# Kernel optimization log

Hardware: AMD Instinct MI355X
Metric: run time of the kernel (lower is better)

## Reference

```python
import jax, jax.numpy as jnp
import numpy as np

D_MODEL = 1024
N_HEADS = 16
D_K = D_MODEL // N_HEADS
SCALE = float(np.sqrt(D_K))


def setup_inputs() -> dict:
    key = jax.random.key(0)
    ks = jax.random.split(key, 12)
    B, S = 2, 2048
    std = 1.0 / np.sqrt(D_MODEL)
    inp = {
        "query": jax.random.normal(ks[0], (B, S, D_MODEL), jnp.float32),
        "key": jax.random.normal(ks[1], (B, S, D_MODEL), jnp.float32),
        "value": jax.random.normal(ks[2], (B, S, D_MODEL), jnp.float32),
        "mask": jnp.ones((B, S), jnp.int32),
        "Wq": jax.random.normal(ks[3], (D_MODEL, D_MODEL), jnp.float32) * std,
        "bq": jnp.zeros((D_MODEL,), jnp.float32),
        "Wk": jax.random.normal(ks[4], (D_MODEL, D_MODEL), jnp.float32) * std,
        "bk": jnp.zeros((D_MODEL,), jnp.float32),
        "Wv": jax.random.normal(ks[5], (D_MODEL, D_MODEL), jnp.float32) * std,
        "bv": jnp.zeros((D_MODEL,), jnp.float32),
        "Wo": jax.random.normal(ks[6], (D_MODEL, D_MODEL), jnp.float32) * std,
        "bo": jnp.zeros((D_MODEL,), jnp.float32),
    }
    return inp


def reference(query, key, value, mask, Wq, bq, Wk, bk, Wv, bv, Wo, bo):
    B, S, _ = query.shape
    # projections -> [B, H, S, d_k]
    def proj(x, W, b):
        return (x @ W.T + b).reshape(B, S, N_HEADS, D_K).transpose(0, 2, 1, 3)

    Q = proj(query, Wq, bq)
    K = proj(key, Wk, bk)
    V = proj(value, Wv, bv)
    # [B, H, Sq, Sk] scores
    scores = jnp.einsum("bhqd,bhkd->bhqk", Q, K) / SCALE
    m = mask[:, None, None, :]  # broadcast over heads and query positions
    scores = jnp.where(m == 0, jnp.float32(-1e9), scores)
    attn = jax.nn.softmax(scores, axis=-1)
    # dropout is identity in eval mode
    context = jnp.einsum("bhqk,bhkd->bhqd", attn, V)
    context = context.transpose(0, 2, 1, 3).reshape(B, S, D_MODEL)
    return context @ Wo.T + bo
```

## Files before the change

### kernel.cpp

```cpp
#include <hip/hip_runtime.h>
#include <stdint.h>

#define D_MODEL 1024
#define NH 16
#define DK 64
#define BATCH 2
#define SEQ 2048
#define MROWS (BATCH*SEQ)

typedef float f32x4 __attribute__((ext_vector_type(4)));
typedef __bf16 bf16x8 __attribute__((ext_vector_type(8)));

#define AS1 __attribute__((address_space(1)))
#define AS3 __attribute__((address_space(3)))

static __device__ __forceinline__ void gld_lds16(const void* g, void* l) {
    __builtin_amdgcn_global_load_lds((const AS1 unsigned int*)g,
                                     (AS3 unsigned int*)l, 16, 0, 0);
}

static __device__ __forceinline__ unsigned int f2bf(float f) {
    union { float f; unsigned int u; } v; v.f = f;
    return (v.u + 0x7fffu + ((v.u >> 16) & 1u)) >> 16;
}

struct PrepArgs {
    const float* src[7];
    unsigned short* dst[7];
    int n4[7];
};

__global__ __launch_bounds__(256) void prep_cvt(PrepArgs a) {
    const int z = blockIdx.y;
    const float4* s = (const float4*)a.src[z];
    ushort4* d = (ushort4*)a.dst[z];
    const int n = a.n4[z];
    for (int i = blockIdx.x * blockDim.x + threadIdx.x; i < n;
         i += gridDim.x * blockDim.x) {
        float4 v = s[i];
        ushort4 o;
        o.x = (unsigned short)f2bf(v.x);
        o.y = (unsigned short)f2bf(v.y);
        o.z = (unsigned short)f2bf(v.z);
        o.w = (unsigned short)f2bf(v.w);
        d[i] = o;
    }
}

struct GemmArgs {
    const unsigned short* A[3];
    const unsigned short* W[3];
    const float* bias[3];
    void* C[3];
    float scale[3];
    int hm[3];
};

template<bool OUT_F32>
__global__ __launch_bounds__(256) void gemm_bt(GemmArgs g) {
    __shared__ unsigned short As[128 * 64];
    __shared__ unsigned short Bs[128 * 64];
    const int z = blockIdx.z;
    const char* A = (const char*)g.A[z];
    const char* W = (const char*)g.W[z];
    const float* bias = g.bias[z];
    const float scale = g.scale[z];
    const int hm = g.hm[z];
    const int t = threadIdx.x;
    const int w = t >> 6, lane = t & 63;
    const int m0 = blockIdx.x * 128, n0 = blockIdx.y * 128;
    const int wm = (w >> 1) * 64, wn = (w & 1) * 64;

    const int srow = t >> 3;
    const int csw = ((t & 7) * 16) ^ ((srow & 7) << 4);
    const char* pA = A + (size_t)(m0 + srow) * 2048 + csw;
    const char* pW = W + (size_t)(n0 + srow) * 2048 + csw;

    f32x4 acc[4][4];
#pragma unroll
    for (int i = 0; i < 4; ++i)
#pragma unroll
        for (int j = 0; j < 4; ++j)
            acc[i][j] = (f32x4){0.f, 0.f, 0.f, 0.f};

    const int kg16 = (lane >> 4) * 16;
    const int swl = (lane & 7) << 4;

    for (int kt = 0; kt < 16; ++kt) {
        __syncthreads();
#pragma unroll
        for (int p = 0; p < 4; ++p) {
            gld_lds16(pA + (size_t)p * (32 * 2048), &As[w * 512 + p * 2048]);
            gld_lds16(pW + (size_t)p * (32 * 2048), &Bs[w * 512 + p * 2048]);
        }
        pA += 128; pW += 128;
        __syncthreads();
#pragma unroll
        for (int ks = 0; ks < 2; ++ks) {
            bf16x8 af[4], bfv[4];
#pragma unroll
            for (int i = 0; i < 4; ++i) {
                int ra = wm + i * 16 + (lane & 15);
                af[i] = *(const bf16x8*)((const char*)As + ra * 128 +
                                         ((ks * 64 + kg16) ^ swl));
                int rb = wn + i * 16 + (lane & 15);
                bfv[i] = *(const bf16x8*)((const char*)Bs + rb * 128 +
                                          ((ks * 64 + kg16) ^ swl));
            }
            __builtin_amdgcn_s_setprio(1);
#pragma unroll
            for (int i = 0; i < 4; ++i)
#pragma unroll
                for (int j = 0; j < 4; ++j)
                    acc[i][j] = __builtin_amdgcn_mfma_f32_16x16x32_bf16(
                        af[i], bfv[j], acc[i][j], 0, 0, 0);
            __builtin_amdgcn_s_setprio(0);
        }
    }

    float bj[4];
#pragma unroll
    for (int j = 0; j < 4; ++j) bj[j] = bias[n0 + wn + j * 16 + (lane & 15)];
#pragma unroll
    for (int i = 0; i < 4; ++i)
#pragma unroll
        for (int r = 0; r < 4; ++r) {
            int row = m0 + wm + i * 16 + (lane >> 4) * 4 + r;
#pragma unroll
            for (int j = 0; j < 4; ++j) {
                int col = n0 + wn + j * 16 + (lane & 15);
                float v = (acc[i][j][r] + bj[j]) * scale;
                if (OUT_F32) {
                    ((float*)g.C[z])[(size_t)row * 1024 + col] = v;
                } else if (hm) {
                    int bb = row >> 11, ss = row & 2047;
                    int hh = col >> 6, dd = col & 63;
                    ((unsigned short*)g.C[z])
                        [(((size_t)(bb * 16 + hh) * 2048) + ss) * 64 + dd] =
                        (unsigned short)f2bf(v);
                } else {
                    ((unsigned short*)g.C[z])[(size_t)row * 1024 + col] =
                        (unsigned short)f2bf(v);
                }
            }
        }
}

__global__ __launch_bounds__(256) void tr_v(
    const unsigned short* __restrict__ Vflat,
    unsigned short* __restrict__ VtT) {
    __shared__ unsigned short T[64 * 66];
    const int bh = blockIdx.y, b = bh >> 4, h = bh & 15;
    const int s0 = blockIdx.x * 64;
    const int t = threadIdx.x, row = t >> 3, ch = t & 7;
#pragma unroll
    for (int p = 0; p < 2; ++p) {
        int r = p * 32 + row;
        const unsigned int* src = (const unsigned int*)(
            Vflat + ((size_t)(b * 2048 + s0 + r) * 1024) + h * 64 + ch * 8);
        unsigned int v0 = src[0], v1 = src[1], v2 = src[2], v3 = src[3];
        unsigned int* dst = (unsigned int*)&T[r * 66 + ch * 8];
        dst[0] = v0; dst[1] = v1; dst[2] = v2; dst[3] = v3;
    }
    __syncthreads();
#pragma unroll
    for (int p = 0; p < 2; ++p) {
        int d = p * 32 + row;
        union { unsigned short u16[8]; uint4 v; } o;
#pragma unroll
        for (int j = 0; j < 8; ++j) o.u16[j] = T[(ch * 8 + j) * 66 + d];
        *(uint4*)(VtT + ((size_t)bh * 64 + d) * 2048 + s0 + ch * 8) = o.v;
    }
}

__global__ __launch_bounds__(256) void attn_fwd(
    const unsigned short* __restrict__ Qh,
    const unsigned short* __restrict__ Kh,
    const unsigned short* __restrict__ VtT,
    const int* __restrict__ mask,
    unsigned short* __restrict__ Ctx) {
    __shared__ unsigned short KlA[4096], KlB[4096];
    __shared__ unsigned short VlA[4096], VlB[4096];
    __shared__ unsigned short Plds[4][2048];

    const int wg = blockIdx.x + (int)gridDim.x * blockIdx.y;
    const int swzid = (wg & 7) * 64 + (wg >> 3);
    const int qt = swzid & 15, bh = swzid >> 4;
    const int b = bh >> 4, h = bh & 15;

    const int t = threadIdx.x, w = t >> 6, lane = t & 63;
    const int wq0 = w * 32;
    const int kg16 = (lane >> 4) * 16;
    const int swl = (lane & 7) << 4;

    const char* Qbase = (const char*)Qh + (size_t)bh * 2048 * 128;
    bf16x8 qf[2][2];
#pragma unroll
    for (int nf = 0; nf < 2; ++nf)
#pragma unroll
        for (int ks = 0; ks < 2; ++ks) {
            int row = qt * 128 + wq0 + nf * 16 + (lane & 15);
            qf[nf][ks] = *(const bf16x8*)(Qbase + (size_t)row * 128 +
                                          ks * 64 + kg16);
        }

    f32x4 cacc[2][4];
#pragma unroll
    for (int i = 0; i < 2; ++i)
#pragma unroll
        for (int j = 0; j < 4; ++j) cacc[i][j] = (f32x4){0.f, 0.f, 0.f, 0.f};
    float mstate[2] = {-3e38f, -3e38f};
    float lstate[2] = {0.f, 0.f};

    const char* Kbyte = (const char*)Kh + (size_t)bh * 2048 * 128;
    const char* Vbyte = (const char*)VtT + (size_t)bh * 64 * 4096;
    const int* mbase = mask + b * SEQ;

    const int srow = t >> 3;
    const int csw = ((t & 7) * 16) ^ ((srow & 7) << 4);
    const size_t srow128 = (size_t)srow * 128;
    const size_t srow4096 = (size_t)srow * 4096;

    auto stage = [&](unsigned short* Kd, unsigned short* Vd, int kv0) {
        const char* ks = Kbyte + (size_t)kv0 * 128;
        gld_lds16(ks + srow128 + csw,               Kd + w * 512);
        gld_lds16(ks + srow128 + 32 * 128 + csw,    Kd + 2048 + w * 512);
        const char* vs = Vbyte + (size_t)kv0 * 2;
        gld_lds16(vs + srow4096 + csw,              Vd + w * 512);
        gld_lds16(vs + srow4096 + 32 * 4096 + csw,  Vd + 2048 + w * 512);
    };

    unsigned short* Pw = &Plds[w][0];

    auto compute = [&](const unsigned short* Kl, const unsigned short* Vl,
                       int kv0) {
        int4 mk[4]; int allone = 1;
#pragma unroll
        for (int mf = 0; mf < 4; ++mf) {
            mk[mf] = *(const int4*)(mbase + kv0 + mf * 16 + (lane >> 4) * 4);
            allone &= (mk[mf].x != 0) & (mk[mf].y != 0) &
                      (mk[mf].z != 0) & (mk[mf].w != 0);
        }

        f32x4 sacc[4][2];
#pragma unroll
        for (int i = 0; i < 4; ++i)
#pragma unroll
            for (int j = 0; j < 2; ++j) sacc[i][j] = (f32x4){0.f, 0.f, 0.f, 0.f};
#pragma unroll
        for (int ks = 0; ks < 2; ++ks) {
            bf16x8 kf[4];
#pragma unroll
            for (int mf = 0; mf < 4; ++mf) {
                int r = mf * 16 + (lane & 15);
                kf[mf] = *(const bf16x8*)((const char*)Kl + r * 128 +
                                          ((ks * 64 + kg16) ^ swl));
            }
            __builtin_amdgcn_s_setprio(1);
#pragma unroll
            for (int mf = 0; mf < 4; ++mf)
#pragma unroll
                for (int nf = 0; nf < 2; ++nf)
                    sacc[mf][nf] = __builtin_amdgcn_mfma_f32_16x16x32_bf16(
                        kf[mf], qf[nf][ks], sacc[mf][nf], 0, 0, 0);
            __builtin_amdgcn_s_setprio(0);
        }

        if (!__all(allone)) {
#pragma unroll
            for (int mf = 0; mf < 4; ++mf)
#pragma unroll
                for (int r = 0; r < 4; ++r) {
                    int mv = (&mk[mf].x)[r];
                    if (mv == 0) {
                        sacc[mf][0][r] = -1e9f;
                        sacc[mf][1][r] = -1e9f;
                    }
                }
        }

        float scalef[2];
#pragma unroll
        for (int nf = 0; nf < 2; ++nf) {
            float a0 = fmaxf(fmaxf(sacc[0][nf][0], sacc[0][nf][1]),
                             fmaxf(sacc[0][nf][2], sacc[0][nf][3]));
            float a1 = fmaxf(fmaxf(sacc[1][nf][0], sacc[1][nf][1]),
                             fmaxf(sacc[1][nf][2], sacc[1][nf][3]));
            float a2 = fmaxf(fmaxf(sacc[2][nf][0], sacc[2][nf][1]),
                             fmaxf(sacc[2][nf][2], sacc[2][nf][3]));
            float a3 = fmaxf(fmaxf(sacc[3][nf][0], sacc[3][nf][1]),
                             fmaxf(sacc[3][nf][2], sacc[3][nf][3]));
            float vm = fmaxf(fmaxf(a0, a1), fmaxf(a2, a3));
            vm = fmaxf(vm, __shfl_xor(vm, 16));
            vm = fmaxf(vm, __shfl_xor(vm, 32));
            float mnew = fmaxf(mstate[nf], vm);
            float sc = __expf(mstate[nf] - mnew);
            scalef[nf] = sc;
            mstate[nf] = mnew;
            float ps[4];
#pragma unroll
            for (int mf = 0; mf < 4; ++mf) {
                float p0 = __expf(sacc[mf][nf][0] - mnew);
                float p1 = __expf(sacc[mf][nf][1] - mnew);
                float p2 = __expf(sacc[mf][nf][2] - mnew);
                float p3 = __expf(sacc[mf][nf][3] - mnew);
                sacc[mf][nf][0] = p0; sacc[mf][nf][1] = p1;
                sacc[mf][nf][2] = p2; sacc[mf][nf][3] = p3;
                ps[mf] = (p0 + p1) + (p2 + p3);
            }
            float s = (ps[0] + ps[1]) + (ps[2] + ps[3]);
            s += __shfl_xor(s, 16);
            s += __shfl_xor(s, 32);
            lstate[nf] = lstate[nf] * sc + s;
        }

#pragma unroll
        for (int mq = 0; mq < 2; ++mq)
#pragma unroll
            for (int r = 0; r < 4; ++r) {
                float sc = __shfl(scalef[mq], (lane >> 4) * 4 + r);
#pragma unroll
                for (int nd = 0; nd < 4; ++nd) cacc[mq][nd][r] *= sc;
            }

#pragma unroll
        for (int nf = 0; nf < 2; ++nf)
#pragma unroll
            for (int mf = 0; mf < 4; ++mf) {
                int q = nf * 16 + (lane & 15);
                int kb = mf * 32 + (lane >> 4) * 8;
                unsigned int p0 = f2bf(sacc[mf][nf][0]) | (f2bf(sacc[mf][nf][1]) << 16);
                unsigned int p1 = f2bf(sacc[mf][nf][2]) | (f2bf(sacc[mf][nf][3]) << 16);
                int sw = (q & 7) << 4;
                *(unsigned int*)((char*)Pw + q * 128 + (kb ^ sw)) = p0;
                *(unsigned int*)((char*)Pw + q * 128 + ((kb + 4) ^ sw)) = p1;
            }

#pragma unroll
        for (int ks = 0; ks < 2; ++ks) {
            bf16x8 pa[2], vf[4];
#pragma unroll
            for (int mq = 0; mq < 2; ++mq) {
                int r = mq * 16 + (lane & 15);
                pa[mq] = *(const bf16x8*)((const char*)Pw + r * 128 +
                                          ((ks * 64 + kg16) ^ swl));
            }
#pragma unroll
            for (int nd = 0; nd < 4; ++nd) {
                int r = nd * 16 + (lane & 15);
                vf[nd] = *(const bf16x8*)((const char*)Vl + r * 128 +
                                          ((ks * 64 + kg16) ^ swl));
            }
            __builtin_amdgcn_s_setprio(1);
#pragma unroll
            for (int mq = 0; mq < 2; ++mq)
#pragma unroll
                for (int nd = 0; nd < 4; ++nd)
                    cacc[mq][nd] = __builtin_amdgcn_mfma_f32_16x16x32_bf16(
                        pa[mq], vf[nd], cacc[mq][nd], 0, 0, 0);
            __builtin_amdgcn_s_setprio(0);
        }
    };

    stage(KlA, VlA, 0);
    __syncthreads();
    for (int i = 0; i < 16; ++i) {
        const int kv0 = i * 128;
        if (kv0 + 64 < SEQ) stage(KlB, VlB, kv0 + 64);
        compute(KlA, VlA, kv0);
        __syncthreads();
        if (kv0 + 128 < SEQ) stage(KlA, VlA, kv0 + 128);
        compute(KlB, VlB, kv0 + 64);
        __syncthreads();
    }

#pragma unroll
    for (int mq = 0; mq < 2; ++mq)
#pragma unroll
        for (int r = 0; r < 4; ++r) {
            float li = __shfl(lstate[mq], (lane >> 4) * 4 + r);
            float inv = 1.f / li;
            size_t row = (size_t)b * SEQ + qt * 128 + wq0 + mq * 16 +
                         (lane >> 4) * 4 + r;
#pragma unroll
            for (int nd = 0; nd < 4; ++nd) {
                int col = h * 64 + nd * 16 + (lane & 15);
                Ctx[row * 1024 + col] = (unsigned short)f2bf(cacc[mq][nd][r] * inv);
            }
        }
}

extern "C" void kernel_launch(void* const* d_in, const int* in_sizes, int n_in,
                              void* d_out, int out_size, void* d_ws, size_t ws_size,
                              hipStream_t stream) {
    const float* q   = (const float*)d_in[0];
    const float* k   = (const float*)d_in[1];
    const float* v   = (const float*)d_in[2];
    const int* mask  = (const int*)d_in[3];
    const float* Wq  = (const float*)d_in[4];
    const float* bq  = (const float*)d_in[5];
    const float* Wk  = (const float*)d_in[6];
    const float* bk  = (const float*)d_in[7];
    const float* Wv  = (const float*)d_in[8];
    const float* bv  = (const float*)d_in[9];
    const float* Wo  = (const float*)d_in[10];
    const float* bo  = (const float*)d_in[11];

    unsigned short* ws = (unsigned short*)d_ws;
    const size_t NX = (size_t)MROWS * D_MODEL;
    const size_t NW = (size_t)D_MODEL * D_MODEL;
    unsigned short* Xq  = ws;
    unsigned short* Xk  = Xq + NX;
    unsigned short* Xv  = Xk + NX;
    unsigned short* Wqb = Xv + NX;
    unsigned short* Wkb = Wqb + NW;
    unsigned short* Wvb = Wkb + NW;
    unsigned short* Wob = Wvb + NW;
    unsigned short* Qhd = Wob + NW;
    unsigned short* Khd = Qhd + NX;
    unsigned short* Vfl = Khd + NX;
    unsigned short* Cx  = Vfl + NX;

    PrepArgs pa;
    pa.src[0] = q;  pa.src[1] = k;  pa.src[2] = v;
    pa.src[3] = Wq; pa.src[4] = Wk; pa.src[5] = Wv; pa.src[6] = Wo;
    pa.dst[0] = Xq;  pa.dst[1] = Xk;  pa.dst[2] = Xv;
    pa.dst[3] = Wqb; pa.dst[4] = Wkb; pa.dst[5] = Wvb; pa.dst[6] = Wob;
    for (int i = 0; i < 3; ++i) pa.n4[i] = (int)(NX / 4);
    for (int i = 3; i < 7; ++i) pa.n4[i] = (int)(NW / 4);
    prep_cvt<<<dim3(256, 7), dim3(256), 0, stream>>>(pa);

    GemmArgs gq;
    gq.A[0] = Xq;  gq.A[1] = Xk;  gq.A[2] = Xv;
    gq.W[0] = Wqb; gq.W[1] = Wkb; gq.W[2] = Wvb;
    gq.bias[0] = bq; gq.bias[1] = bk; gq.bias[2] = bv;
    gq.C[0] = Qhd; gq.C[1] = Khd; gq.C[2] = Vfl;
    gq.scale[0] = 0.125f; gq.scale[1] = 1.f; gq.scale[2] = 1.f;
    gq.hm[0] = 1; gq.hm[1] = 1; gq.hm[2] = 0;
    gemm_bt<false><<<dim3(32, 8, 3), dim3(256), 0, stream>>>(gq);

    tr_v<<<dim3(32, 32), dim3(256), 0, stream>>>(Vfl, Xv);

    attn_fwd<<<dim3(16, 32), dim3(256), 0, stream>>>(Qhd, Khd, Xv, mask, Cx);

    GemmArgs go;
    go.A[0] = Cx; go.W[0] = Wob; go.bias[0] = bo; go.C[0] = d_out;
    go.scale[0] = 1.f; go.hm[0] = 0;
    go.A[1] = go.A[2] = nullptr; go.W[1] = go.W[2] = nullptr;
    go.bias[1] = go.bias[2] = nullptr; go.C[1] = go.C[2] = nullptr;
    go.scale[1] = go.scale[2] = 1.f; go.hm[1] = go.hm[2] = 0;
    gemm_bt<true><<<dim3(32, 8, 1), dim3(256), 0, stream>>>(go);
}
```

Baseline: 263.3 us.

## Fuse V transpose into projection GEMM and streamline attention softmax

The V projection GEMM now writes its output directly in the transposed per-head layout, which removes the separate transpose kernel and its extra pass over memory. The attention kernel checks the mask once per block and skips per-tile masking when every key is valid. It folds log2(e) into the Q scale so it can use exp2. It skips rescaling the running state unless the max grows by more than a threshold, and it computes the row sums with an MFMA against a ones vector. Other changes use hardware bf16 conversion with packed stores and give the output GEMM a narrower N tile to launch more blocks, at the cost of more complex code and slightly different rounding behaviour.

```diff
diff --git a/kernel.cpp b/kernel.cpp
--- a/kernel.cpp
+++ b/kernel.cpp
@@ -14,14 +14,27 @@
 #define AS1 __attribute__((address_space(1)))
 #define AS3 __attribute__((address_space(3)))
 
+#if __has_builtin(__builtin_amdgcn_exp2f)
+#define EXP2F(x) __builtin_amdgcn_exp2f(x)
+#else
+#define EXP2F(x) exp2f(x)
+#endif
+#if __has_builtin(__builtin_amdgcn_rcpf)
+#define RCPF(x) __builtin_amdgcn_rcpf(x)
+#else
+#define RCPF(x) (1.0f/(x))
+#endif
+
 static __device__ __forceinline__ void gld_lds16(const void* g, void* l) {
     __builtin_amdgcn_global_load_lds((const AS1 unsigned int*)g,
                                      (AS3 unsigned int*)l, 16, 0, 0);
 }
 
-static __device__ __forceinline__ unsigned int f2bf(float f) {
-    union { float f; unsigned int u; } v; v.f = f;
-    return (v.u + 0x7fffu + ((v.u >> 16) & 1u)) >> 16;
+static __device__ __forceinline__ unsigned short bfbits(float f) {
+    return __builtin_bit_cast(unsigned short, (__bf16)f);
+}
+static __device__ __forceinline__ unsigned int pk2bf(float a, float b) {
+    return (unsigned int)bfbits(a) | ((unsigned int)bfbits(b) << 16);
 }
 
 struct PrepArgs {
@@ -33,16 +46,14 @@
 __global__ __launch_bounds__(256) void prep_cvt(PrepArgs a) {
     const int z = blockIdx.y;
     const float4* s = (const float4*)a.src[z];
-    ushort4* d = (ushort4*)a.dst[z];
+    uint2* d = (uint2*)a.dst[z];
     const int n = a.n4[z];
     for (int i = blockIdx.x * blockDim.x + threadIdx.x; i < n;
          i += gridDim.x * blockDim.x) {
         float4 v = s[i];
-        ushort4 o;
-        o.x = (unsigned short)f2bf(v.x);
-        o.y = (unsigned short)f2bf(v.y);
-        o.z = (unsigned short)f2bf(v.z);
-        o.w = (unsigned short)f2bf(v.w);
+        uint2 o;
+        o.x = pk2bf(v.x, v.y);
+        o.y = pk2bf(v.z, v.w);
         d[i] = o;
     }
 }
@@ -56,10 +67,11 @@
     int hm[3];
 };
 
-template<bool OUT_F32>
+template<bool OUT_F32, int BN>
 __global__ __launch_bounds__(256) void gemm_bt(GemmArgs g) {
+    constexpr int JN = BN / 32;
     __shared__ unsigned short As[128 * 64];
-    __shared__ unsigned short Bs[128 * 64];
+    __shared__ unsigned short Bs[BN * 64];
     const int z = blockIdx.z;
     const char* A = (const char*)g.A[z];
     const char* W = (const char*)g.W[z];
@@ -68,19 +80,19 @@
     const int hm = g.hm[z];
     const int t = threadIdx.x;
     const int w = t >> 6, lane = t & 63;
-    const int m0 = blockIdx.x * 128, n0 = blockIdx.y * 128;
-    const int wm = (w >> 1) * 64, wn = (w & 1) * 64;
+    const int m0 = blockIdx.x * 128, n0 = blockIdx.y * BN;
+    const int wm = (w >> 1) * 64, wn = (w & 1) * (BN / 2);
 
     const int srow = t >> 3;
     const int csw = ((t & 7) * 16) ^ ((srow & 7) << 4);
     const char* pA = A + (size_t)(m0 + srow) * 2048 + csw;
     const char* pW = W + (size_t)(n0 + srow) * 2048 + csw;
 
-    f32x4 acc[4][4];
+    f32x4 acc[4][JN];
 #pragma unroll
     for (int i = 0; i < 4; ++i)
 #pragma unroll
-        for (int j = 0; j < 4; ++j)
+        for (int j = 0; j < JN; ++j)
             acc[i][j] = (f32x4){0.f, 0.f, 0.f, 0.f};
 
     const int kg16 = (lane >> 4) * 16;
@@ -89,45 +101,71 @@
     for (int kt = 0; kt < 16; ++kt) {
         __syncthreads();
 #pragma unroll
-        for (int p = 0; p < 4; ++p) {
+        for (int p = 0; p < 4; ++p)
             gld_lds16(pA + (size_t)p * (32 * 2048), &As[w * 512 + p * 2048]);
+#pragma unroll
+        for (int p = 0; p < JN; ++p)
             gld_lds16(pW + (size_t)p * (32 * 2048), &Bs[w * 512 + p * 2048]);
-        }
         pA += 128; pW += 128;
         __syncthreads();
 #pragma unroll
         for (int ks = 0; ks < 2; ++ks) {
-            bf16x8 af[4], bfv[4];
+            bf16x8 af[4], bfv[JN];
 #pragma unroll
             for (int i = 0; i < 4; ++i) {
                 int ra = wm + i * 16 + (lane & 15);
                 af[i] = *(const bf16x8*)((const char*)As + ra * 128 +
                                          ((ks * 64 + kg16) ^ swl));
-                int rb = wn + i * 16 + (lane & 15);
-                bfv[i] = *(const bf16x8*)((const char*)Bs + rb * 128 +
+            }
+#pragma unroll
+            for (int j = 0; j < JN; ++j) {
+                int rb = wn + j * 16 + (lane & 15);
+                bfv[j] = *(const bf16x8*)((const char*)Bs + rb * 128 +
                                           ((ks * 64 + kg16) ^ swl));
             }
             __builtin_amdgcn_s_setprio(1);
 #pragma unroll
             for (int i = 0; i < 4; ++i)
 #pragma unroll
-                for (int j = 0; j < 4; ++j)
+                for (int j = 0; j < JN; ++j)
                     acc[i][j] = __builtin_amdgcn_mfma_f32_16x16x32_bf16(
                         af[i], bfv[j], acc[i][j], 0, 0, 0);
             __builtin_amdgcn_s_setprio(0);
         }
     }
 
-    float bj[4];
-#pragma unroll
-    for (int j = 0; j < 4; ++j) bj[j] = bias[n0 + wn + j * 16 + (lane & 15)];
+    float bj[JN];
+#pragma unroll
+    for (int j = 0; j < JN; ++j) bj[j] = bias[n0 + wn + j * 16 + (lane & 15)];
+
+    if (hm == 2) {
+#pragma unroll
+        for (int i = 0; i < 4; ++i) {
+            int row0 = m0 + wm + i * 16 + ((lane >> 4) << 2);
+            int bb = row0 >> 11, ss0 = row0 & 2047;
+#pragma unroll
+            for (int j = 0; j < JN; ++j) {
+                int col = n0 + wn + j * 16 + (lane & 15);
+                int hh = col >> 6, dd = col & 63;
+                ushort4 o;
+                o.x = bfbits(acc[i][j][0] + bj[j]);
+                o.y = bfbits(acc[i][j][1] + bj[j]);
+                o.z = bfbits(acc[i][j][2] + bj[j]);
+                o.w = bfbits(acc[i][j][3] + bj[j]);
+                *(ushort4*)((unsigned short*)g.C[z] +
+                            (((size_t)(bb * 16 + hh) * 64 + dd) * 2048 + ss0)) = o;
+            }
+        }
+        return;
+    }
+
 #pragma unroll
     for (int i = 0; i < 4; ++i)
 #pragma unroll
         for (int r = 0; r < 4; ++r) {
             int row = m0 + wm + i * 16 + (lane >> 4) * 4 + r;
 #pragma unroll
-            for (int j = 0; j < 4; ++j) {
+            for (int j = 0; j < JN; ++j) {
                 int col = n0 + wn + j * 16 + (lane & 15);
                 float v = (acc[i][j][r] + bj[j]) * scale;
                 if (OUT_F32) {
@@ -137,40 +175,13 @@
                     int hh = col >> 6, dd = col & 63;
                     ((unsigned short*)g.C[z])
                         [(((size_t)(bb * 16 + hh) * 2048) + ss) * 64 + dd] =
-                        (unsigned short)f2bf(v);
+                        bfbits(v);
                 } else {
                     ((unsigned short*)g.C[z])[(size_t)row * 1024 + col] =
-                        (unsigned short)f2bf(v);
+                        bfbits(v);
                 }
             }
         }
-}
-
-__global__ __launch_bounds__(256) void tr_v(
-    const unsigned short* __restrict__ Vflat,
-    unsigned short* __restrict__ VtT) {
-    __shared__ unsigned short T[64 * 66];
-    const int bh = blockIdx.y, b = bh >> 4, h = bh & 15;
-    const int s0 = blockIdx.x * 64;
-    const int t = threadIdx.x, row = t >> 3, ch = t & 7;
-#pragma unroll
-    for (int p = 0; p < 2; ++p) {
-        int r = p * 32 + row;
-        const unsigned int* src = (const unsigned int*)(
-            Vflat + ((size_t)(b * 2048 + s0 + r) * 1024) + h * 64 + ch * 8);
-        unsigned int v0 = src[0], v1 = src[1], v2 = src[2], v3 = src[3];
-        unsigned int* dst = (unsigned int*)&T[r * 66 + ch * 8];
-        dst[0] = v0; dst[1] = v1; dst[2] = v2; dst[3] = v3;
-    }
-    __syncthreads();
-#pragma unroll
-    for (int p = 0; p < 2; ++p) {
-        int d = p * 32 + row;
-        union { unsigned short u16[8]; uint4 v; } o;
-#pragma unroll
-        for (int j = 0; j < 8; ++j) o.u16[j] = T[(ch * 8 + j) * 66 + d];
-        *(uint4*)(VtT + ((size_t)bh * 64 + d) * 2048 + s0 + ch * 8) = o.v;
-    }
 }
 
 __global__ __launch_bounds__(256) void attn_fwd(
@@ -182,6 +193,7 @@
     __shared__ unsigned short KlA[4096], KlB[4096];
     __shared__ unsigned short VlA[4096], VlB[4096];
     __shared__ unsigned short Plds[4][2048];
+    __shared__ int cfl[4];
 
     const int wg = blockIdx.x + (int)gridDim.x * blockIdx.y;
     const int swzid = (wg & 7) * 64 + (wg >> 3);
@@ -190,8 +202,19 @@
 
     const int t = threadIdx.x, w = t >> 6, lane = t & 63;
     const int wq0 = w * 32;
-    const int kg16 = (lane >> 4) * 16;
+    const int g = lane >> 4;
+    const int kg16 = g * 16;
     const int swl = (lane & 7) << 4;
+
+    const int* mbase = mask + b * SEQ;
+    int myclean = 1;
+#pragma unroll
+    for (int i = 0; i < 2; ++i) {
+        int4 m4 = ((const int4*)mbase)[t + i * 256];
+        myclean &= (m4.x != 0) & (m4.y != 0) & (m4.z != 0) & (m4.w != 0);
+    }
+    int wc = __all(myclean);
+    if (lane == 0) cfl[w] = wc;
 
     const char* Qbase = (const char*)Qh + (size_t)bh * 2048 * 128;
     bf16x8 qf[2][2];
@@ -204,17 +227,21 @@
                                           ks * 64 + kg16);
         }
 
-    f32x4 cacc[2][4];
-#pragma unroll
-    for (int i = 0; i < 2; ++i)
+    bf16x8 onesf;
+#pragma unroll
+    for (int j = 0; j < 8; ++j) onesf[j] = (__bf16)1.0f;
+
+    f32x4 cacc[2][4], lacc[2];
+#pragma unroll
+    for (int i = 0; i < 2; ++i) {
+        lacc[i] = (f32x4){0.f, 0.f, 0.f, 0.f};
 #pragma unroll
         for (int j = 0; j < 4; ++j) cacc[i][j] = (f32x4){0.f, 0.f, 0.f, 0.f};
+    }
     float mstate[2] = {-3e38f, -3e38f};
-    float lstate[2] = {0.f, 0.f};
 
     const char* Kbyte = (const char*)Kh + (size_t)bh * 2048 * 128;
     const char* Vbyte = (const char*)VtT + (size_t)bh * 64 * 4096;
-    const int* mbase = mask + b * SEQ;
 
     const int srow = t >> 3;
     const int csw = ((t & 7) * 16) ^ ((srow & 7) << 4);
@@ -230,18 +257,13 @@
         gld_lds16(vs + srow4096 + 32 * 4096 + csw,  Vd + 2048 + w * 512);
     };
 
+    __syncthreads();
+    const int clean = cfl[0] & cfl[1] & cfl[2] & cfl[3];
+
     unsigned short* Pw = &Plds[w][0];
 
     auto compute = [&](const unsigned short* Kl, const unsigned short* Vl,
                        int kv0) {
-        int4 mk[4]; int allone = 1;
-#pragma unroll
-        for (int mf = 0; mf < 4; ++mf) {
-            mk[mf] = *(const int4*)(mbase + kv0 + mf * 16 + (lane >> 4) * 4);
-            allone &= (mk[mf].x != 0) & (mk[mf].y != 0) &
-                      (mk[mf].z != 0) & (mk[mf].w != 0);
-        }
-
         f32x4 sacc[4][2];
 #pragma unroll
         for (int i = 0; i < 4; ++i)
@@ -266,20 +288,21 @@
             __builtin_amdgcn_s_setprio(0);
         }
 
-        if (!__all(allone)) {
-#pragma unroll
-            for (int mf = 0; mf < 4; ++mf)
+        if (!clean) {
+#pragma unroll
+            for (int mf = 0; mf < 4; ++mf) {
+                int4 mk = *(const int4*)(mbase + kv0 + mf * 16 + g * 4);
 #pragma unroll
                 for (int r = 0; r < 4; ++r) {
-                    int mv = (&mk[mf].x)[r];
-                    if (mv == 0) {
+                    if ((&mk.x)[r] == 0) {
                         sacc[mf][0][r] = -1e9f;
                         sacc[mf][1][r] = -1e9f;
                     }
                 }
-        }
-
-        float scalef[2];
+            }
+        }
+
+        float vm[2];
 #pragma unroll
         for (int nf = 0; nf < 2; ++nf) {
             float a0 = fmaxf(fmaxf(sacc[0][nf][0], sacc[0][nf][1]),
@@ -290,51 +313,46 @@
                              fmaxf(sacc[2][nf][2], sacc[2][nf][3]));
             float a3 = fmaxf(fmaxf(sacc[3][nf][0], sacc[3][nf][1]),
                              fmaxf(sacc[3][nf][2], sacc[3][nf][3]));
-            float vm = fmaxf(fmaxf(a0, a1), fmaxf(a2, a3));
-            vm = fmaxf(vm, __shfl_xor(vm, 16));
-            vm = fmaxf(vm, __shfl_xor(vm, 32));
-            float mnew = fmaxf(mstate[nf], vm);
-            float sc = __expf(mstate[nf] - mnew);
-            scalef[nf] = sc;
-            mstate[nf] = mnew;
-            float ps[4];
+            float m4 = fmaxf(fmaxf(a0, a1), fmaxf(a2, a3));
+            m4 = fmaxf(m4, __shfl_xor(m4, 16));
+            vm[nf] = fmaxf(m4, __shfl_xor(m4, 32));
+        }
+        if (!__all((vm[0] <= mstate[0] + 8.f) & (vm[1] <= mstate[1] + 8.f))) {
+            float sc[2];
+#pragma unroll
+            for (int nf = 0; nf < 2; ++nf) {
+                float mnew = fmaxf(mstate[nf], vm[nf]);
+                sc[nf] = EXP2F(mstate[nf] - mnew);
+                mstate[nf] = mnew;
+            }
+#pragma unroll
+            for (int mq = 0; mq < 2; ++mq)
+#pragma unroll
+                for (int r = 0; r < 4; ++r) {
+                    float scb = __shfl(sc[mq], g * 4 + r);
+                    lacc[mq][r] *= scb;
+#pragma unroll
+                    for (int nd = 0; nd < 4; ++nd) cacc[mq][nd][r] *= scb;
+                }
+        }
+
+#pragma unroll
+        for (int nf = 0; nf < 2; ++nf) {
+            float mn = mstate[nf];
 #pragma unroll
             for (int mf = 0; mf < 4; ++mf) {
-                float p0 = __expf(sacc[mf][nf][0] - mnew);
-                float p1 = __expf(sacc[mf][nf][1] - mnew);
-                float p2 = __expf(sacc[mf][nf][2] - mnew);
-                float p3 = __expf(sacc[mf][nf][3] - mnew);
-                sacc[mf][nf][0] = p0; sacc[mf][nf][1] = p1;
-                sacc[mf][nf][2] = p2; sacc[mf][nf][3] = p3;
-                ps[mf] = (p0 + p1) + (p2 + p3);
-            }
-            float s = (ps[0] + ps[1]) + (ps[2] + ps[3]);
-            s += __shfl_xor(s, 16);
-            s += __shfl_xor(s, 32);
-            lstate[nf] = lstate[nf] * sc + s;
-        }
-
-#pragma unroll
-        for (int mq = 0; mq < 2; ++mq)
-#pragma unroll
-            for (int r = 0; r < 4; ++r) {
-                float sc = __shfl(scalef[mq], (lane >> 4) * 4 + r);
-#pragma unroll
-                for (int nd = 0; nd < 4; ++nd) cacc[mq][nd][r] *= sc;
-            }
-
-#pragma unroll
-        for (int nf = 0; nf < 2; ++nf)
-#pragma unroll
-            for (int mf = 0; mf < 4; ++mf) {
+                unsigned int d0 = pk2bf(EXP2F(sacc[mf][nf][0] - mn),
+                                        EXP2F(sacc[mf][nf][1] - mn));
+                unsigned int d1 = pk2bf(EXP2F(sacc[mf][nf][2] - mn),
+                                        EXP2F(sacc[mf][nf][3] - mn));
                 int q = nf * 16 + (lane & 15);
-                int kb = mf * 32 + (lane >> 4) * 8;
-                unsigned int p0 = f2bf(sacc[mf][nf][0]) | (f2bf(sacc[mf][nf][1]) << 16);
-                unsigned int p1 = f2bf(sacc[mf][nf][2]) | (f2bf(sacc[mf][nf][3]) << 16);
-                int sw = (q & 7) << 4;
-                *(unsigned int*)((char*)Pw + q * 128 + (kb ^ sw)) = p0;
-                *(unsigned int*)((char*)Pw + q * 128 + ((kb + 4) ^ sw)) = p1;
-            }
+                int kb = mf * 32 + g * 8;
+                unsigned long long pv =
+                    (unsigned long long)d0 | ((unsigned long long)d1 << 32);
+                *(unsigned long long*)((char*)Pw + q * 128 +
+                                       (kb ^ ((q & 7) << 4))) = pv;
+            }
+        }
 
 #pragma unroll
         for (int ks = 0; ks < 2; ++ks) {
@@ -353,11 +371,14 @@
             }
             __builtin_amdgcn_s_setprio(1);
 #pragma unroll
-            for (int mq = 0; mq < 2; ++mq)
+            for (int mq = 0; mq < 2; ++mq) {
+                lacc[mq] = __builtin_amdgcn_mfma_f32_16x16x32_bf16(
+                    pa[mq], onesf, lacc[mq], 0, 0, 0);
 #pragma unroll
                 for (int nd = 0; nd < 4; ++nd)
                     cacc[mq][nd] = __builtin_amdgcn_mfma_f32_16x16x32_bf16(
                         pa[mq], vf[nd], cacc[mq][nd], 0, 0, 0);
+            }
             __builtin_amdgcn_s_setprio(0);
         }
     };
@@ -378,14 +399,13 @@
     for (int mq = 0; mq < 2; ++mq)
 #pragma unroll
         for (int r = 0; r < 4; ++r) {
-            float li = __shfl(lstate[mq], (lane >> 4) * 4 + r);
-            float inv = 1.f / li;
+            float inv = RCPF(lacc[mq][r]);
             size_t row = (size_t)b * SEQ + qt * 128 + wq0 + mq * 16 +
-                         (lane >> 4) * 4 + r;
+                         g * 4 + r;
 #pragma unroll
             for (int nd = 0; nd < 4; ++nd) {
                 int col = h * 64 + nd * 16 + (lane & 15);
-                Ctx[row * 1024 + col] = (unsigned short)f2bf(cacc[mq][nd][r] * inv);
+                Ctx[row * 1024 + col] = bfbits(cacc[mq][nd][r] * inv);
             }
         }
 }
@@ -418,8 +438,8 @@
     unsigned short* Wob = Wvb + NW;
     unsigned short* Qhd = Wob + NW;
     unsigned short* Khd = Qhd + NX;
-    unsigned short* Vfl = Khd + NX;
-    unsigned short* Cx  = Vfl + NX;
+    unsigned short* Vtt = Khd + NX;
+    unsigned short* Cx  = Vtt + NX;
 
     PrepArgs pa;
     pa.src[0] = q;  pa.src[1] = k;  pa.src[2] = v;
@@ -434,14 +454,13 @@
     gq.A[0] = Xq;  gq.A[1] = Xk;  gq.A[2] = Xv;
     gq.W[0] = Wqb; gq.W[1] = Wkb; gq.W[2] = Wvb;
     gq.bias[0] = bq; gq.bias[1] = bk; gq.bias[2] = bv;
-    gq.C[0] = Qhd; gq.C[1] = Khd; gq.C[2] = Vfl;
-    gq.scale[0] = 0.125f; gq.scale[1] = 1.f; gq.scale[2] = 1.f;
-    gq.hm[0] = 1; gq.hm[1] = 1; gq.hm[2] = 0;
-    gemm_bt<false><<<dim3(32, 8, 3), dim3(256), 0, stream>>>(gq);
-
-    tr_v<<<dim3(32, 32), dim3(256), 0, stream>>>(Vfl, Xv);
-
-    attn_fwd<<<dim3(16, 32), dim3(256), 0, stream>>>(Qhd, Khd, Xv, mask, Cx);
+    gq.C[0] = Qhd; gq.C[1] = Khd; gq.C[2] = Vtt;
+    gq.scale[0] = 0.125f * 1.44269504088896340736f;
+    gq.scale[1] = 1.f; gq.scale[2] = 1.f;
+    gq.hm[0] = 1; gq.hm[1] = 1; gq.hm[2] = 2;
+    gemm_bt<false, 128><<<dim3(32, 8, 3), dim3(256), 0, stream>>>(gq);
+
+    attn_fwd<<<dim3(16, 32), dim3(256), 0, stream>>>(Qhd, Khd, Vtt, mask, Cx);
 
     GemmArgs go;
     go.A[0] = Cx; go.W[0] = Wob; go.bias[0] = bo; go.C[0] = d_out;
@@ -449,5 +468,5 @@
     go.A[1] = go.A[2] = nullptr; go.W[1] = go.W[2] = nullptr;
     go.bias[1] = go.bias[2] = nullptr; go.C[1] = go.C[2] = nullptr;
     go.scale[1] = go.scale[2] = 1.f; go.hm[1] = go.hm[2] = 0;
-    gemm_bt<true><<<dim3(32, 8, 1), dim3(256), 0, stream>>>(go);
-}
+    gemm_bt<true, 64><<<dim3(32, 16, 1), dim3(256), 0, stream>>>(go);
+}
```

New measurement: 227.8 us. 13.5% less time.
